# Performance work log

Hardware: AMD Instinct MI355X
Metric: run time of the kernel (lower is better)

Reference implementation:

```python
import jax, jax.numpy as jnp
import numpy as np

B, C, D, N, NCLS = 2048, 96, 384, 200000, 10
LN_EPS = 1e-5


def setup_inputs() -> dict:
    key = jax.random.key(0)
    ks = jax.random.split(key, 16)
    s = 0.05  # keep squared-distance logits in a sane range
    inp = {
        'k': jax.random.normal(ks[0], (B, D), jnp.float32) * s,
        'context_idx': jax.random.randint(ks[1], (B, C), 0, N),
        'candidate_embeddings': jax.random.normal(ks[2], (N, D), jnp.float32) * s,
        'candidate_y': jax.random.randint(ks[3], (N,), 0, NCLS),
        # learned params
        'label_emb': jax.random.normal(ks[4], (NCLS, D), jnp.float32) * 0.02,
        'ln_g': jnp.ones((D,), jnp.float32),
        'ln_b': jnp.zeros((D,), jnp.float32),
        'kp_w1': jax.random.normal(ks[5], (D, D), jnp.float32) * (1.0 / np.sqrt(D)),
        'kp_b1': jnp.zeros((D,), jnp.float32),
        'kp_w2': jax.random.normal(ks[6], (D, D), jnp.float32) * (1.0 / np.sqrt(D)),
        'kp_b2': jnp.zeros((D,), jnp.float32),
        'pw1': jax.random.normal(ks[7], (D, D), jnp.float32) * (1.0 / np.sqrt(D)),
        'pb1': jnp.zeros((D,), jnp.float32),
        'pw2': jax.random.normal(ks[8], (D, NCLS), jnp.float32) * (1.0 / np.sqrt(D)),
        'pb2': jnp.zeros((NCLS,), jnp.float32),
    }
    return inp


def reference(k, context_idx, candidate_embeddings, candidate_y,
              label_emb, ln_g, ln_b, kp_w1, kp_b1, kp_w2, kp_b2,
              pw1, pb1, pw2, pb2):
    # gather context (irregular access): [B, C, D], [B, C]
    context_k = candidate_embeddings[context_idx]
    context_y = candidate_y[context_idx]

    # negative squared distance via kernel trick: -|k|^2 + 2 k.ck - |ck|^2
    sim = (-jnp.sum(k * k, axis=-1, keepdims=True)
           + 2.0 * jnp.einsum('bd,bcd->bc', k, context_k)
           - jnp.sum(context_k * context_k, axis=-1))  # [B, C]
    probs = jax.nn.softmax(sim, axis=-1)  # dropout is identity in eval mode

    context_y_emb = label_emb[context_y]  # [B, C, D]

    # key_proj: LayerNorm -> Linear -> SiLU -> Linear, residual (d_main==n_out)
    def key_proj(x):
        mu = jnp.mean(x, axis=-1, keepdims=True)
        var = jnp.mean(jnp.square(x - mu), axis=-1, keepdims=True)
        h = (x - mu) * jax.lax.rsqrt(var + LN_EPS) * ln_g + ln_b
        h = jax.nn.silu(h @ kp_w1 + kp_b1)
        h = h @ kp_w2 + kp_b2
        return x + h

    # Abl == -1 branch: values = label_emb + key_proj(k - context_k)
    values = context_y_emb + key_proj(k[:, None, :] - context_k)  # [B, C, D]

    # probs[:, None] @ values -> weighted sum over context
    context_x = jnp.einsum('bc,bcd->bd', probs, values)
    x = k + context_x

    # predictor MLP (no residual: d_main != n_classes)
    h = jax.nn.silu(x @ pw1 + pb1)
    y = h @ pw2 + pb2
    return y
```

## Files before the change

kernel.cpp:

```cpp
#include <hip/hip_runtime.h>
#include <hip/hip_bf16.h>

#define BB   2048
#define CC   96
#define DD   384
#define NCLSS 10
#define AS_STRIDE 392

typedef __attribute__((ext_vector_type(8))) __bf16 bf16x8;
typedef __attribute__((ext_vector_type(4))) float  floatx4;
typedef unsigned int  uint32;
typedef unsigned short ushort16;

__device__ __forceinline__ float bflo(uint32 u){ return __uint_as_float(u << 16); }
__device__ __forceinline__ float bfhi(uint32 u){ return __uint_as_float(u & 0xffff0000u); }
__device__ __forceinline__ float bf1(ushort16 s){ return __uint_as_float(((uint32)s) << 16); }
__device__ __forceinline__ ushort16 f2bf(float f){
  uint32 u = __float_as_uint(f);
  return (ushort16)((u + 0x7fffu + ((u >> 16) & 1u)) >> 16);
}
__device__ __forceinline__ int probe_f32(const void* lng_raw){
  return (((const uint32*)lng_raw)[0] == 0x3F800000u) ? 1 : 0;
}
__device__ __forceinline__ float ld1(const void* p, size_t i, int isf32){
  return isf32 ? ((const float*)p)[i] : bf1(((const ushort16*)p)[i]);
}
__device__ __forceinline__ void ld6(const void* base, size_t row_elems, int lane, int isf32, float v[6]){
  if (isf32){
    const float2* p = (const float2*)((const float*)base + row_elems) + (size_t)lane*3;
    float2 a = p[0], b = p[1], c = p[2];
    v[0]=a.x; v[1]=a.y; v[2]=b.x; v[3]=b.y; v[4]=c.x; v[5]=c.y;
  } else {
    const uint32* p = (const uint32*)((const ushort16*)base + row_elems) + (size_t)lane*3;
    uint32 a = p[0], b = p[1], c = p[2];
    v[0]=bflo(a); v[1]=bfhi(a); v[2]=bflo(b); v[3]=bfhi(b); v[4]=bflo(c); v[5]=bfhi(c);
  }
}

__global__ __launch_bounds__(256) void k_canon(
    const void* w1, const void* w2, const void* pw1, const void* lng,
    ushort16* __restrict__ wW1T, ushort16* __restrict__ wW2T,
    ushort16* __restrict__ wPW1T)
{
  int isf32 = probe_f32(lng);
  int m  = blockIdx.x / 144;
  int t  = blockIdx.x % 144;
  int tr = t / 12, tc = t % 12;
  const void* src = (m == 0) ? w1 : (m == 1) ? w2 : pw1;
  ushort16* dst   = (m == 0) ? wW1T : (m == 1) ? wW2T : wPW1T;
  __shared__ float tile[32][33];
  int tx = threadIdx.x & 31, ty = threadIdx.x >> 5;
  #pragma unroll
  for (int p = 0; p < 4; p++)
    tile[p*8 + ty][tx] = ld1(src, (size_t)(tr*32 + p*8 + ty) * DD + tc*32 + tx, isf32);
  __syncthreads();
  #pragma unroll
  for (int p = 0; p < 4; p++)
    dst[(size_t)(tc*32 + p*8 + ty) * DD + tr*32 + tx] = f2bf(tile[tx][p*8 + ty]);
}

__device__ __forceinline__ void store_row(
    int c, const float dv[6], float mu, float rsig,
    const float gv[6], const float bvv[6], ushort16* As, int lane)
{
  uint32 wa[3];
  #pragma unroll
  for (int p = 0; p < 3; p++) {
    float a0 = (dv[2*p]   - mu) * rsig * gv[2*p]   + bvv[2*p];
    float a1 = (dv[2*p+1] - mu) * rsig * gv[2*p+1] + bvv[2*p+1];
    wa[p] = (uint32)f2bf(a0) | ((uint32)f2bf(a1) << 16);
  }
  uint32* ap = (uint32*)As + c * (AS_STRIDE/2) + lane * 3;
  ap[0] = wa[0]; ap[1] = wa[1]; ap[2] = wa[2];
}

__device__ __forceinline__ void process_pair(
    int c0, const float a[6], const float b[6],
    const float kv[6], const float gv[6], const float bvv[6],
    ushort16* As, float* sims, float* muv, float* sigv, int lane)
{
  float da[6], db[6];
  float s1a=0.f, s2a=0.f, s1b=0.f, s2b=0.f;
  #pragma unroll
  for (int j = 0; j < 6; j++) {
    da[j] = kv[j] - a[j]; s1a += da[j]; s2a += da[j]*da[j];
    db[j] = kv[j] - b[j]; s1b += db[j]; s2b += db[j]*db[j];
  }
  #pragma unroll
  for (int m = 32; m; m >>= 1) {
    s1a += __shfl_xor(s1a, m); s2a += __shfl_xor(s2a, m);
    s1b += __shfl_xor(s1b, m); s2b += __shfl_xor(s2b, m);
  }
  float mua = s1a * (1.f/DD), vara = s2a * (1.f/DD) - mua*mua;
  float mub = s1b * (1.f/DD), varb = s2b * (1.f/DD) - mub*mub;
  float rsa = rsqrtf(vara + 1e-5f), rsb = rsqrtf(varb + 1e-5f);
  if (lane == 0) {
    sims[c0] = -s2a;   muv[c0] = mua;   sigv[c0] = sqrtf(vara + 1e-5f);
    sims[c0+1] = -s2b; muv[c0+1] = mub; sigv[c0+1] = sqrtf(varb + 1e-5f);
  }
  store_row(c0,   da, mua, rsa, gv, bvv, As, lane);
  store_row(c0+1, db, mub, rsb, gv, bvv, As, lane);
}

__global__ __launch_bounds__(512, 4) void k_fused(
    const void* kptr, const int* __restrict__ cidx,
    const void* cand, const int* __restrict__ cy,
    const void* lng, const void* lnb, const void* b1,
    const ushort16* __restrict__ w1t,
    float* __restrict__ wxpre, float* __restrict__ wpl, float* __restrict__ wsum)
{
  int isf32 = probe_f32(lng);
  int b = blockIdx.x;
  int tid = threadIdx.x, wave = tid >> 6, lane = tid & 63;
  __shared__ __align__(16) ushort16 As[CC * AS_STRIDE];
  __shared__ float sims[CC], probs[CC], muv[CC], sigv[CC];
  __shared__ float plbuf[NCLSS], xacc[DD], sacc[2];

  if (tid < NCLSS) plbuf[tid] = 0.f;
  if (tid < DD)    xacc[tid]  = 0.f;
  if (tid < 2)     sacc[tid]  = 0.f;

  float kv[6], gv[6], bvv[6];
  ld6(kptr, (size_t)b * DD, lane, isf32, kv);
  ld6(lng, 0, lane, isf32, gv);
  ld6(lnb, 0, lane, isf32, bvv);

  int idxs[12];
  #pragma unroll
  for (int t = 0; t < 12; t++) idxs[t] = cidx[b * CC + wave * 12 + t];

  float cva[2][6], cvb[2][6];
  ld6(cand, (size_t)idxs[0] * DD, lane, isf32, cva[0]);
  ld6(cand, (size_t)idxs[1] * DD, lane, isf32, cvb[0]);
  #pragma unroll 1
  for (int ip = 0; ip < 6; ip++) {
    int cur = ip & 1, nxt = cur ^ 1;
    if (ip < 5) {
      ld6(cand, (size_t)idxs[2*ip+2] * DD, lane, isf32, cva[nxt]);
      ld6(cand, (size_t)idxs[2*ip+3] * DD, lane, isf32, cvb[nxt]);
    }
    process_pair(wave*12 + 2*ip, cva[cur], cvb[cur], kv, gv, bvv,
                 As, sims, muv, sigv, lane);
  }
  __syncthreads();

  if (wave == 0) {
    float v0 = sims[lane];
    float v1 = (lane < 32) ? sims[lane + 64] : -1e30f;
    float mx = fmaxf(v0, v1);
    #pragma unroll
    for (int m = 32; m; m >>= 1) mx = fmaxf(mx, __shfl_xor(mx, m));
    float e0 = __expf(v0 - mx);
    float e1 = (lane < 32) ? __expf(v1 - mx) : 0.f;
    float s = e0 + e1;
    #pragma unroll
    for (int m = 32; m; m >>= 1) s += __shfl_xor(s, m);
    float inv = 1.f / s;
    probs[lane] = e0 * inv;
    if (lane < 32) probs[lane + 64] = e1 * inv;
  }
  __syncthreads();

  if (tid < CC) atomicAdd(&plbuf[cy[cidx[b * CC + tid]]], probs[tid]);
  {
    float T0=0,T1=0,T2=0,T3=0,T4=0,T5=0, S1p=0, Smup=0;
    #pragma unroll
    for (int i = 0; i < 12; i++) {
      int c = wave * 12 + i;
      float p = probs[c], ps = p * sigv[c];
      const uint32* ap = (const uint32*)As + c * (AS_STRIDE/2) + lane * 3;
      uint32 a0 = ap[0], a1 = ap[1], a2 = ap[2];
      T0 += ps*bflo(a0); T1 += ps*bfhi(a0); T2 += ps*bflo(a1);
      T3 += ps*bfhi(a1); T4 += ps*bflo(a2); T5 += ps*bfhi(a2);
      S1p += ps; Smup += p * muv[c];
    }
    int j0 = lane * 6;
    atomicAdd(&xacc[j0+0], T0); atomicAdd(&xacc[j0+1], T1);
    atomicAdd(&xacc[j0+2], T2); atomicAdd(&xacc[j0+3], T3);
    atomicAdd(&xacc[j0+4], T4); atomicAdd(&xacc[j0+5], T5);
    if (lane == 0) { atomicAdd(&sacc[0], S1p); atomicAdd(&sacc[1], Smup); }
  }
  __syncthreads();

  if (tid < DD) {
    float gj = ld1(lng, tid, isf32), bj = ld1(lnb, tid, isf32);
    wxpre[(size_t)b * DD + tid] =
        ld1(kptr, (size_t)b * DD + tid, isf32)
        + (xacc[tid] - bj * sacc[0]) / gj + sacc[1];
  }
  if (tid < NCLSS) wpl[b * NCLSS + tid] = plbuf[tid];

  int col = lane & 15, quad = lane >> 4;
  int n0 = wave * 48;
  floatx4 acc[6][3];
  #pragma unroll
  for (int i = 0; i < 6; i++)
    #pragma unroll
    for (int j = 0; j < 3; j++) acc[i][j] = (floatx4)0.f;

  const ushort16* wbase = w1t + (size_t)(n0 + col) * DD + quad * 8;
  bf16x8 bcur[3];
  #pragma unroll
  for (int tn = 0; tn < 3; tn++)
    bcur[tn] = *(const bf16x8*)(wbase + (size_t)tn * 16 * DD);
  #pragma unroll 1
  for (int kt = 0; kt < 12; kt++) {
    bf16x8 bnxt[3];
    if (kt < 11) {
      #pragma unroll
      for (int tn = 0; tn < 3; tn++)
        bnxt[tn] = *(const bf16x8*)(wbase + (size_t)tn * 16 * DD + (kt+1) * 32);
    }
    #pragma unroll
    for (int tm = 0; tm < 6; tm++) {
      bf16x8 afrag = *(const bf16x8*)(As + (tm*16 + col) * AS_STRIDE + kt*32 + quad*8);
      #pragma unroll
      for (int tn = 0; tn < 3; tn++)
        acc[tm][tn] = __builtin_amdgcn_mfma_f32_16x16x32_bf16(afrag, bcur[tn], acc[tm][tn], 0, 0, 0);
    }
    #pragma unroll
    for (int tn = 0; tn < 3; tn++) bcur[tn] = bnxt[tn];
  }

  #pragma unroll
  for (int tn = 0; tn < 3; tn++) {
    int n = n0 + tn*16 + col;
    float bias = ld1(b1, n, isf32);
    float val = 0.f;
    #pragma unroll
    for (int tm = 0; tm < 6; tm++) {
      #pragma unroll
      for (int r = 0; r < 4; r++) {
        int row = tm*16 + quad*4 + r;
        float h = acc[tm][tn][r] + bias;
        h = h / (1.f + __expf(-h));
        val += probs[row] * h;
      }
    }
    val += __shfl_xor(val, 16);
    val += __shfl_xor(val, 32);
    if (quad == 0) wsum[(size_t)b * DD + n] = val;
  }
}

__global__ __launch_bounds__(512) void k_final(
    const float* __restrict__ wxpre, const float* __restrict__ wsum,
    const float* __restrict__ wpl, const void* lemb,
    const ushort16* __restrict__ w2t, const void* b2,
    const ushort16* __restrict__ pw1t, const void* pb1,
    const void* pw2, const void* pb2,
    const void* lng_raw, void* out)
{
  int isf32 = probe_f32(lng_raw);
  int b0 = blockIdx.x * 8;
  int tid = threadIdx.x, wave = tid >> 6, lane = tid & 63;
  int cn = lane & 15, quad = lane >> 4;
  __shared__ __align__(16) ushort16 As[16 * AS_STRIDE];
  __shared__ float hbuf[8][AS_STRIDE];
  __shared__ float lembsh[NCLSS * DD];
  __shared__ float plsh[8][NCLSS];
  __shared__ float part[480];

  for (int e = tid; e < 16 * AS_STRIDE; e += 512) {
    int r = e / AS_STRIDE, j = e - r * AS_STRIDE;
    ushort16 v = (ushort16)0;
    if (r < 8 && j < DD) v = f2bf(wsum[(size_t)(b0 + r) * DD + j]);
    As[e] = v;
  }
  for (int e = tid; e < NCLSS * DD; e += 512) lembsh[e] = ld1(lemb, e, isf32);
  if (tid < 80) plsh[tid / NCLSS][tid % NCLSS] = wpl[(b0 + tid / NCLSS) * NCLSS + tid % NCLSS];
  __syncthreads();

  int n0 = wave * 48;
  floatx4 acc[3];
  #pragma unroll
  for (int j = 0; j < 3; j++) acc[j] = (floatx4)0.f;
  const ushort16* wb2 = w2t + (size_t)(n0 + cn) * DD + quad * 8;
  #pragma unroll 2
  for (int kt = 0; kt < 12; kt++) {
    bf16x8 afrag = *(const bf16x8*)(As + cn * AS_STRIDE + kt*32 + quad*8);
    #pragma unroll
    for (int tn = 0; tn < 3; tn++) {
      bf16x8 bfrag = *(const bf16x8*)(wb2 + (size_t)tn * 16 * DD + kt * 32);
      acc[tn] = __builtin_amdgcn_mfma_f32_16x16x32_bf16(afrag, bfrag, acc[tn], 0, 0, 0);
    }
  }
  float xv[3][4];
  #pragma unroll
  for (int tn = 0; tn < 3; tn++) {
    int n = n0 + tn*16 + cn;
    float bb = ld1(b2, n, isf32);
    #pragma unroll
    for (int r = 0; r < 4; r++) {
      int row = quad*4 + r;
      if (row < 8) {
        float v = acc[tn][r] + bb + wxpre[(size_t)(b0 + row) * DD + n];
        #pragma unroll
        for (int l = 0; l < NCLSS; l++) v += plsh[row][l] * lembsh[l * DD + n];
        xv[tn][r] = v;
      }
    }
  }
  __syncthreads();
  #pragma unroll
  for (int tn = 0; tn < 3; tn++) {
    int n = n0 + tn*16 + cn;
    #pragma unroll
    for (int r = 0; r < 4; r++) {
      int row = quad*4 + r;
      if (row < 8) As[row * AS_STRIDE + n] = f2bf(xv[tn][r]);
    }
  }
  __syncthreads();

  floatx4 acc2[3];
  #pragma unroll
  for (int j = 0; j < 3; j++) acc2[j] = (floatx4)0.f;
  const ushort16* wbp = pw1t + (size_t)(n0 + cn) * DD + quad * 8;
  #pragma unroll 2
  for (int kt = 0; kt < 12; kt++) {
    bf16x8 afrag = *(const bf16x8*)(As + cn * AS_STRIDE + kt*32 + quad*8);
    #pragma unroll
    for (int tn = 0; tn < 3; tn++) {
      bf16x8 bfrag = *(const bf16x8*)(wbp + (size_t)tn * 16 * DD + kt * 32);
      acc2[tn] = __builtin_amdgcn_mfma_f32_16x16x32_bf16(afrag, bfrag, acc2[tn], 0, 0, 0);
    }
  }
  #pragma unroll
  for (int tn = 0; tn < 3; tn++) {
    int n = n0 + tn*16 + cn;
    float bb = ld1(pb1, n, isf32);
    #pragma unroll
    for (int r = 0; r < 4; r++) {
      int row = quad*4 + r;
      if (row < 8) {
        float h = acc2[tn][r] + bb;
        hbuf[row][n] = h / (1.f + __expf(-h));
      }
    }
  }
  __syncthreads();

  if (tid < 480) {
    int r = tid / 60, rem = tid % 60, n = rem / 6, s = rem % 6;
    float pp = 0.f;
    int jb = s * 64;
    #pragma unroll 8
    for (int jj = 0; jj < 64; jj++) {
      int j = jb + jj;
      pp += hbuf[r][j] * ld1(pw2, (size_t)j * NCLSS + n, isf32);
    }
    part[tid] = pp;
  }
  __syncthreads();
  if (tid < 80) {
    int r = tid / NCLSS, n = tid % NCLSS;
    float y = ld1(pb2, n, isf32);
    #pragma unroll
    for (int s = 0; s < 6; s++) y += part[r*60 + n*6 + s];
    size_t o = (size_t)(b0 + r) * NCLSS + n;
    if (isf32) ((float*)out)[o] = y;
    else       ((ushort16*)out)[o] = f2bf(y);
  }
}

extern "C" void kernel_launch(void* const* d_in, const int* in_sizes, int n_in,
                              void* d_out, int out_size, void* d_ws, size_t ws_size,
                              hipStream_t stream) {
  const void* kptr = d_in[0];
  const int*  cidx = (const int*)d_in[1];
  const void* cand = d_in[2];
  const int*  cy   = (const int*)d_in[3];
  const void* lemb = d_in[4];
  const void* lng  = d_in[5];
  const void* lnb  = d_in[6];
  const void* w1   = d_in[7];
  const void* b1   = d_in[8];
  const void* w2   = d_in[9];
  const void* b2   = d_in[10];
  const void* pw1  = d_in[11];
  const void* pb1  = d_in[12];
  const void* pw2  = d_in[13];
  const void* pb2  = d_in[14];

  char* ws = (char*)d_ws;
  ushort16* wW1T  = (ushort16*)(ws);
  ushort16* wW2T  = (ushort16*)(ws + 294912);
  ushort16* wPW1T = (ushort16*)(ws + 589824);
  float*    wxpre = (float*)   (ws + 884736);
  float*    wpl   = (float*)   (ws + 4030464);
  float*    wsum  = (float*)   (ws + 4112384);

  k_canon<<<432, 256, 0, stream>>>(w1, w2, pw1, lng, wW1T, wW2T, wPW1T);
  k_fused<<<BB, 512, 0, stream>>>(kptr, cidx, cand, cy, lng, lnb, b1, wW1T,
                                  wxpre, wpl, wsum);
  k_final<<<256, 512, 0, stream>>>(wxpre, wsum, wpl, lemb, wW2T, b2,
                                   wPW1T, pb1, pw2, pb2, lng, d_out);
}
```

Before: 600.0 us.

## Restructure context gather/LayerNorm into MFMA-fragment layout with XOR-swizzled LDS

Replaces the per-wave, row-at-a-time gather and LayerNorm (each lane owning 6 contiguous elements, 64-lane reductions) with a mapping where 16-lane groups each own one context row and lanes load 8-element vectors matching the MFMA k-chunks. The A-tile in shared memory drops the padded stride for a dense 768-byte row with an XOR swizzle, meant to avoid bank conflicts on both the vector stores and the MFMA fragment reads. The candidate row is read twice (once for statistics, once for normalisation), and 4 of 16 lane groups do redundant work because only 12 rows map per wave. This trades extra global or L2 traffic and wasted lanes for wider loads and cheaper reductions.

```diff
diff --git a/kernel.cpp b/kernel.cpp
--- a/kernel.cpp
+++ b/kernel.cpp
@@ -11,6 +11,7 @@
 typedef __attribute__((ext_vector_type(4))) float  floatx4;
 typedef unsigned int  uint32;
 typedef unsigned short ushort16;
+typedef __attribute__((ext_vector_type(4))) uint32 uintx4;
 
 __device__ __forceinline__ float bflo(uint32 u){ return __uint_as_float(u << 16); }
 __device__ __forceinline__ float bfhi(uint32 u){ return __uint_as_float(u & 0xffff0000u); }
@@ -25,15 +26,16 @@
 __device__ __forceinline__ float ld1(const void* p, size_t i, int isf32){
   return isf32 ? ((const float*)p)[i] : bf1(((const ushort16*)p)[i]);
 }
-__device__ __forceinline__ void ld6(const void* base, size_t row_elems, int lane, int isf32, float v[6]){
+__device__ __forceinline__ void ld8(const void* base, size_t eoff, int isf32, float v[8]){
   if (isf32){
-    const float2* p = (const float2*)((const float*)base + row_elems) + (size_t)lane*3;
-    float2 a = p[0], b = p[1], c = p[2];
-    v[0]=a.x; v[1]=a.y; v[2]=b.x; v[3]=b.y; v[4]=c.x; v[5]=c.y;
+    const floatx4* p = (const floatx4*)((const float*)base + eoff);
+    floatx4 a = p[0], b = p[1];
+    v[0]=a[0]; v[1]=a[1]; v[2]=a[2]; v[3]=a[3];
+    v[4]=b[0]; v[5]=b[1]; v[6]=b[2]; v[7]=b[3];
   } else {
-    const uint32* p = (const uint32*)((const ushort16*)base + row_elems) + (size_t)lane*3;
-    uint32 a = p[0], b = p[1], c = p[2];
-    v[0]=bflo(a); v[1]=bfhi(a); v[2]=bflo(b); v[3]=bfhi(b); v[4]=bflo(c); v[5]=bfhi(c);
+    uintx4 a = *(const uintx4*)((const ushort16*)base + eoff);
+    v[0]=bflo(a[0]); v[1]=bfhi(a[0]); v[2]=bflo(a[1]); v[3]=bfhi(a[1]);
+    v[4]=bflo(a[2]); v[5]=bfhi(a[2]); v[6]=bflo(a[3]); v[7]=bfhi(a[3]);
   }
 }
 
@@ -59,49 +61,6 @@
     dst[(size_t)(tc*32 + p*8 + ty) * DD + tr*32 + tx] = f2bf(tile[tx][p*8 + ty]);
 }
 
-__device__ __forceinline__ void store_row(
-    int c, const float dv[6], float mu, float rsig,
-    const float gv[6], const float bvv[6], ushort16* As, int lane)
-{
-  uint32 wa[3];
-  #pragma unroll
-  for (int p = 0; p < 3; p++) {
-    float a0 = (dv[2*p]   - mu) * rsig * gv[2*p]   + bvv[2*p];
-    float a1 = (dv[2*p+1] - mu) * rsig * gv[2*p+1] + bvv[2*p+1];
-    wa[p] = (uint32)f2bf(a0) | ((uint32)f2bf(a1) << 16);
-  }
-  uint32* ap = (uint32*)As + c * (AS_STRIDE/2) + lane * 3;
-  ap[0] = wa[0]; ap[1] = wa[1]; ap[2] = wa[2];
-}
-
-__device__ __forceinline__ void process_pair(
-    int c0, const float a[6], const float b[6],
-    const float kv[6], const float gv[6], const float bvv[6],
-    ushort16* As, float* sims, float* muv, float* sigv, int lane)
-{
-  float da[6], db[6];
-  float s1a=0.f, s2a=0.f, s1b=0.f, s2b=0.f;
-  #pragma unroll
-  for (int j = 0; j < 6; j++) {
-    da[j] = kv[j] - a[j]; s1a += da[j]; s2a += da[j]*da[j];
-    db[j] = kv[j] - b[j]; s1b += db[j]; s2b += db[j]*db[j];
-  }
-  #pragma unroll
-  for (int m = 32; m; m >>= 1) {
-    s1a += __shfl_xor(s1a, m); s2a += __shfl_xor(s2a, m);
-    s1b += __shfl_xor(s1b, m); s2b += __shfl_xor(s2b, m);
-  }
-  float mua = s1a * (1.f/DD), vara = s2a * (1.f/DD) - mua*mua;
-  float mub = s1b * (1.f/DD), varb = s2b * (1.f/DD) - mub*mub;
-  float rsa = rsqrtf(vara + 1e-5f), rsb = rsqrtf(varb + 1e-5f);
-  if (lane == 0) {
-    sims[c0] = -s2a;   muv[c0] = mua;   sigv[c0] = sqrtf(vara + 1e-5f);
-    sims[c0+1] = -s2b; muv[c0+1] = mub; sigv[c0+1] = sqrtf(varb + 1e-5f);
-  }
-  store_row(c0,   da, mua, rsa, gv, bvv, As, lane);
-  store_row(c0+1, db, mub, rsb, gv, bvv, As, lane);
-}
-
 __global__ __launch_bounds__(512, 4) void k_fused(
     const void* kptr, const int* __restrict__ cidx,
     const void* cand, const int* __restrict__ cy,
@@ -112,7 +71,8 @@
   int isf32 = probe_f32(lng);
   int b = blockIdx.x;
   int tid = threadIdx.x, wave = tid >> 6, lane = tid & 63;
-  __shared__ __align__(16) ushort16 As[CC * AS_STRIDE];
+  int t = lane & 15, kq = lane >> 4;
+  __shared__ __align__(16) char AsB[96 * 768];
   __shared__ float sims[CC], probs[CC], muv[CC], sigv[CC];
   __shared__ float plbuf[NCLSS], xacc[DD], sacc[2];
 
@@ -120,27 +80,46 @@
   if (tid < DD)    xacc[tid]  = 0.f;
   if (tid < 2)     sacc[tid]  = 0.f;
 
-  float kv[6], gv[6], bvv[6];
-  ld6(kptr, (size_t)b * DD, lane, isf32, kv);
-  ld6(lng, 0, lane, isf32, gv);
-  ld6(lnb, 0, lane, isf32, bvv);
-
-  int idxs[12];
-  #pragma unroll
-  for (int t = 0; t < 12; t++) idxs[t] = cidx[b * CC + wave * 12 + t];
-
-  float cva[2][6], cvb[2][6];
-  ld6(cand, (size_t)idxs[0] * DD, lane, isf32, cva[0]);
-  ld6(cand, (size_t)idxs[1] * DD, lane, isf32, cvb[0]);
-  #pragma unroll 1
-  for (int ip = 0; ip < 6; ip++) {
-    int cur = ip & 1, nxt = cur ^ 1;
-    if (ip < 5) {
-      ld6(cand, (size_t)idxs[2*ip+2] * DD, lane, isf32, cva[nxt]);
-      ld6(cand, (size_t)idxs[2*ip+3] * DD, lane, isf32, cvb[nxt]);
-    }
-    process_pair(wave*12 + 2*ip, cva[cur], cvb[cur], kv, gv, bvv,
-                 As, sims, muv, sigv, lane);
+  int tr = (t < 12) ? t : t - 12;
+  int c  = wave * 12 + tr;
+  int idx = cidx[b * CC + c];
+
+  float s1 = 0.f, s2 = 0.f;
+  #pragma unroll
+  for (int kt = 0; kt < 12; kt++) {
+    int j0 = kt * 32 + kq * 8;
+    float ck[8], kk[8];
+    ld8(cand, (size_t)idx * DD + j0, isf32, ck);
+    ld8(kptr, (size_t)b   * DD + j0, isf32, kk);
+    #pragma unroll
+    for (int j = 0; j < 8; j++) { float d = kk[j] - ck[j]; s1 += d; s2 += d * d; }
+  }
+  s1 += __shfl_xor(s1, 16); s2 += __shfl_xor(s2, 16);
+  s1 += __shfl_xor(s1, 32); s2 += __shfl_xor(s2, 32);
+  float mu = s1 * (1.f/DD), var = s2 * (1.f/DD) - mu*mu;
+  float rsig = rsqrtf(var + 1e-5f);
+  if (kq == 0 && t < 12) { sims[c] = -s2; muv[c] = mu; sigv[c] = sqrtf(var + 1e-5f); }
+
+  int swz = (c & 7) << 4;
+  #pragma unroll 4
+  for (int kt = 0; kt < 12; kt++) {
+    int j0 = kt * 32 + kq * 8;
+    float ck[8], kk[8], g8[8], h8[8];
+    ld8(cand, (size_t)idx * DD + j0, isf32, ck);
+    ld8(kptr, (size_t)b   * DD + j0, isf32, kk);
+    ld8(lng, j0, isf32, g8);
+    ld8(lnb, j0, isf32, h8);
+    uint32 w[4];
+    #pragma unroll
+    for (int p = 0; p < 4; p++) {
+      float a0 = (kk[2*p]   - ck[2*p]   - mu) * rsig * g8[2*p]   + h8[2*p];
+      float a1 = (kk[2*p+1] - ck[2*p+1] - mu) * rsig * g8[2*p+1] + h8[2*p+1];
+      w[p] = (uint32)f2bf(a0) | ((uint32)f2bf(a1) << 16);
+    }
+    if (t < 12) {
+      uintx4 vv = { w[0], w[1], w[2], w[3] };
+      *(uintx4*)(AsB + ((c * 768 + kt * 64 + kq * 16) ^ swz)) = vv;
+    }
   }
   __syncthreads();
 
@@ -166,13 +145,16 @@
     float T0=0,T1=0,T2=0,T3=0,T4=0,T5=0, S1p=0, Smup=0;
     #pragma unroll
     for (int i = 0; i < 12; i++) {
-      int c = wave * 12 + i;
-      float p = probs[c], ps = p * sigv[c];
-      const uint32* ap = (const uint32*)As + c * (AS_STRIDE/2) + lane * 3;
-      uint32 a0 = ap[0], a1 = ap[1], a2 = ap[2];
+      int cc = wave * 12 + i;
+      float p = probs[cc], ps = p * sigv[cc];
+      const char* rp = AsB + cc * 768;
+      int sz = (cc & 7) << 4;
+      uint32 a0 = *(const uint32*)(rp + ((lane*12 + 0) ^ sz));
+      uint32 a1 = *(const uint32*)(rp + ((lane*12 + 4) ^ sz));
+      uint32 a2 = *(const uint32*)(rp + ((lane*12 + 8) ^ sz));
       T0 += ps*bflo(a0); T1 += ps*bfhi(a0); T2 += ps*bflo(a1);
       T3 += ps*bfhi(a1); T4 += ps*bflo(a2); T5 += ps*bfhi(a2);
-      S1p += ps; Smup += p * muv[c];
+      S1p += ps; Smup += p * muv[cc];
     }
     int j0 = lane * 6;
     atomicAdd(&xacc[j0+0], T0); atomicAdd(&xacc[j0+1], T1);
@@ -205,7 +187,7 @@
     bcur[tn] = *(const bf16x8*)(wbase + (size_t)tn * 16 * DD);
   #pragma unroll 1
   for (int kt = 0; kt < 12; kt++) {
-    bf16x8 bnxt[3];
+    bf16x8 bnxt[3] = { (bf16x8)0, (bf16x8)0, (bf16x8)0 };
     if (kt < 11) {
       #pragma unroll
       for (int tn = 0; tn < 3; tn++)
@@ -213,7 +195,8 @@
     }
     #pragma unroll
     for (int tm = 0; tm < 6; tm++) {
-      bf16x8 afrag = *(const bf16x8*)(As + (tm*16 + col) * AS_STRIDE + kt*32 + quad*8);
+      int r = tm*16 + col;
+      bf16x8 afrag = *(const bf16x8*)(AsB + ((r * 768 + kt*64 + quad*16) ^ ((r & 7) << 4)));
       #pragma unroll
       for (int tn = 0; tn < 3; tn++)
         acc[tm][tn] = __builtin_amdgcn_mfma_f32_16x16x32_bf16(afrag, bcur[tn], acc[tm][tn], 0, 0, 0);
```

After: 800.8 us. 33.5% more time.
